# Kernel tuning notes

Measured on AMD Instinct MI355X. Metric: run time of the kernel, lower is better.

Reference implementation:

```python
import jax, jax.numpy as jnp
import numpy as np
import math

EMBED_DIM = 1024
N_HEADS = 16
HEAD_DIM = EMBED_DIM // N_HEADS  # 64


def setup_inputs() -> dict:
    key = jax.random.key(0)
    k1, k2, k3, k4, k5 = jax.random.split(key, 5)
    B, N, D, H, hd = 2, 2048, EMBED_DIM, N_HEADS, HEAD_DIM
    x = jax.random.normal(k1, (B, N, D), dtype=jnp.float32)
    # per-head kqv Linear weights, stacked: [H, D, 3*hd] (in->out layout)
    scale_in = 1.0 / math.sqrt(D)
    Wqkv = jax.random.uniform(k2, (H, D, 3 * hd), minval=-scale_in, maxval=scale_in, dtype=jnp.float32)
    bqkv = jax.random.uniform(k3, (H, 3 * hd), minval=-scale_in, maxval=scale_in, dtype=jnp.float32)
    # output projection: [D, D] (in->out layout) + bias [D]
    Wo = jax.random.uniform(k4, (D, D), minval=-scale_in, maxval=scale_in, dtype=jnp.float32)
    bo = jax.random.uniform(k5, (D,), minval=-scale_in, maxval=scale_in, dtype=jnp.float32)
    return {"x": x, "Wqkv": Wqkv, "bqkv": bqkv, "Wo": Wo, "bo": bo}


def reference(x, Wqkv, bqkv, Wo, bo):
    B, N, D = x.shape
    H, _, _ = Wqkv.shape
    hd = D // H
    # fused per-head QKV projections: [B, H, N, 3*hd]
    qkv = jnp.einsum('bnd,hdk->bhnk', x, Wqkv) + bqkv[None, :, None, :]
    k, q, v = jnp.split(qkv, 3, axis=-1)  # chunk order in source is k, q, v
    # scores: A = q @ k^T / sqrt(head_dim)  -> [B, H, N, N]
    scores = jnp.einsum('bhqd,bhkd->bhqk', q, k) / math.sqrt(hd)
    causal = jnp.tril(jnp.ones((N, N), dtype=bool))
    scores = jnp.where(causal[None, None, :, :], scores, -jnp.inf)
    attn = jax.nn.softmax(scores, axis=-1)
    sa = jnp.einsum('bhqk,bhkd->bhqd', attn, v)  # [B, H, N, hd]
    # concat heads -> [B, N, D]
    sa = sa.transpose(0, 2, 1, 3).reshape(B, N, D)
    return sa @ Wo + bo
```

## Files before the change

### kernel.cpp

```cpp
#include <hip/hip_runtime.h>
#include <stdint.h>

typedef unsigned short u16;
typedef short s16x8 __attribute__((ext_vector_type(8)));
typedef unsigned short u16x8 __attribute__((ext_vector_type(8)));
typedef unsigned int u32x4 __attribute__((ext_vector_type(4)));
typedef float f32x4 __attribute__((ext_vector_type(4)));
typedef float f32x16 __attribute__((ext_vector_type(16)));

#define GLD16(g, l) __builtin_amdgcn_global_load_lds( \
    (const __attribute__((address_space(1))) uint32_t*)(g), \
    (__attribute__((address_space(3))) uint32_t*)(l), 16, 0, 0)

__device__ __forceinline__ u16 f2bf(float f) {
  uint32_t u = __builtin_bit_cast(uint32_t, f);
  u += 0x7fffu + ((u >> 16) & 1u);
  return (u16)(u >> 16);
}

__device__ __forceinline__ uint32_t cvtpk(float lo, float hi) {
  uint32_t r;
  asm("v_cvt_pk_bf16_f32 %0, %1, %2" : "=v"(r) : "v"(lo), "v"(hi));
  return r;
}

__global__ void cvt_kernel(const float* __restrict__ in, u16* __restrict__ out) {
  int i = blockIdx.x * 256 + threadIdx.x;
  const float4* p = (const float4*)in + (size_t)i * 2;
  float4 a = p[0], b = p[1];
  u16x8 o;
  o[0] = f2bf(a.x); o[1] = f2bf(a.y); o[2] = f2bf(a.z); o[3] = f2bf(a.w);
  o[4] = f2bf(b.x); o[5] = f2bf(b.y); o[6] = f2bf(b.z); o[7] = f2bf(b.w);
  *((u16x8*)out + i) = o;
}

__global__ void transpose_f2b(const float* __restrict__ in, u16* __restrict__ out,
                              int R, int C) {
  __shared__ float tile[32][33];
  const int bz = blockIdx.z;
  in  += (size_t)bz * R * C;
  out += (size_t)bz * R * C;
  int c0 = blockIdx.x * 32, r0 = blockIdx.y * 32;
  int tx = threadIdx.x, ty = threadIdx.y;
  #pragma unroll
  for (int i = 0; i < 32; i += 8)
    tile[ty + i][tx] = in[(size_t)(r0 + ty + i) * C + c0 + tx];
  __syncthreads();
  #pragma unroll
  for (int i = 0; i < 32; i += 8)
    out[(size_t)(c0 + ty + i) * R + r0 + tx] = f2bf(tile[tx][ty + i]);
}

__global__ void transpose_b2b(const u16* __restrict__ in, u16* __restrict__ out,
                              int R, int C) {
  __shared__ u16 tile[32][33];
  const int bz = blockIdx.z;
  in  += (size_t)bz * R * C;
  out += (size_t)bz * R * C;
  int c0 = blockIdx.x * 32, r0 = blockIdx.y * 32;
  int tx = threadIdx.x, ty = threadIdx.y;
  #pragma unroll
  for (int i = 0; i < 32; i += 8)
    tile[ty + i][tx] = in[(size_t)(r0 + ty + i) * C + c0 + tx];
  __syncthreads();
  #pragma unroll
  for (int i = 0; i < 32; i += 8)
    out[(size_t)(c0 + ty + i) * R + r0 + tx] = tile[tx][ty + i];
}

template <int EPI>
__global__ __launch_bounds__(256) void gemm128(
    const u16* __restrict__ A, const u16* __restrict__ Bt, int K,
    const float* __restrict__ bias,
    u16* __restrict__ kb, u16* __restrict__ qb, u16* __restrict__ vb,
    float* __restrict__ fout) {
  __shared__ __align__(16) u16 As[128 * 64];
  __shared__ __align__(16) u16 Bs[128 * 64];
  const int tid = threadIdx.x;
  const int lane = tid & 63;
  const int wr = (tid >> 6) >> 1, wc = (tid >> 6) & 1;
  const int row0 = blockIdx.y * 128, col0 = blockIdx.x * 128;
  const int l15 = lane & 15, l4 = lane >> 4;
  const u16* Ablk = A + (size_t)row0 * K;
  const u16* Bblk = Bt + (size_t)col0 * K;
  f32x4 acc[4][4] = {};
  for (int k0 = 0; k0 < K; k0 += 64) {
    #pragma unroll
    for (int i = 0; i < 4; i++) {
      int off = (i * 256 + tid) * 8;
      int r = off >> 6, c = off & 63;
      GLD16(Ablk + (size_t)r * K + k0 + c, As + off);
    }
    #pragma unroll
    for (int i = 0; i < 4; i++) {
      int off = (i * 256 + tid) * 8;
      int r = off >> 6, c = off & 63;
      GLD16(Bblk + (size_t)r * K + k0 + c, Bs + off);
    }
    __syncthreads();
    #pragma unroll
    for (int kc = 0; kc < 2; kc++) {
      s16x8 af[4], bfr[4];
      #pragma unroll
      for (int m = 0; m < 4; m++)
        af[m] = *(const s16x8*)(As + (wr * 64 + m * 16 + l15) * 64 + kc * 32 + l4 * 8);
      #pragma unroll
      for (int n = 0; n < 4; n++)
        bfr[n] = *(const s16x8*)(Bs + (wc * 64 + n * 16 + l15) * 64 + kc * 32 + l4 * 8);
      #pragma unroll
      for (int m = 0; m < 4; m++)
        #pragma unroll
        for (int n = 0; n < 4; n++)
          acc[m][n] = __builtin_amdgcn_mfma_f32_16x16x32_bf16(af[m], bfr[n], acc[m][n], 0, 0, 0);
    }
    __syncthreads();
  }
  const int rbase = row0 + wr * 64;
  const int cbase = col0 + wc * 64;
  if (EPI == 0) {
    #pragma unroll
    for (int n = 0; n < 4; n++) {
      int c = cbase + n * 16 + l15;
      int h = c / 192, rr = c % 192;
      int part = rr >> 6, d = rr & 63;
      float bv = bias[h * 192 + rr];
      u16* dst = (part == 0) ? kb : (part == 1) ? qb : vb;
      float sc = (part == 1) ? 0.125f * 1.44269504f : 1.0f;
      #pragma unroll
      for (int m = 0; m < 4; m++)
        #pragma unroll
        for (int i = 0; i < 4; i++) {
          int r = rbase + m * 16 + l4 * 4 + i;
          int b = r >> 11, nn = r & 2047;
          dst[(((size_t)(b * 16 + h) * 2048 + nn) << 6) + d] = f2bf((acc[m][n][i] + bv) * sc);
        }
    }
  } else {
    #pragma unroll
    for (int n = 0; n < 4; n++) {
      int c = cbase + n * 16 + l15;
      float bv = bias[c];
      #pragma unroll
      for (int m = 0; m < 4; m++)
        #pragma unroll
        for (int i = 0; i < 4; i++) {
          int r = rbase + m * 16 + l4 * 4 + i;
          fout[(size_t)r * 1024 + c] = acc[m][n][i] + bv;
        }
    }
  }
}

__global__ __launch_bounds__(256, 2) void attn_kernel(
    const u16* __restrict__ q, const u16* __restrict__ k,
    const u16* __restrict__ vt, u16* __restrict__ sa) {
  __shared__ __align__(16) u16 Ks[2][64 * 64];
  __shared__ __align__(16) u16 Vs[2][64 * 64];
  __shared__ __align__(16) float Mo[2][64][36];
  __shared__ float Mml[2][64][2];
  const int tid = threadIdx.x;
  const int lane = tid & 63;
  const int wave = tid >> 6;
  const int p = wave & 1;
  const int q2 = wave >> 1;
  const int l31 = lane & 31;
  const int h = lane >> 5;

  const int bid = blockIdx.x;
  const int bh = (bid & 7) * 4 + ((bid >> 3) & 3);
  const int j = bid >> 5;
  const u16* kbh = k + (((size_t)bh * 2048) << 6);
  const u16* vbh = vt + (size_t)bh * 64 * 2048;
  const int b_ = bh >> 4, head = bh & 15;
  const int swz = (l31 & 7) << 4;

  int cur = 0;
  for (int sub = 0; sub < 2; sub++) {
    const int t = sub ? j : (31 - j);
    const int qrow = t * 64 + p * 32 + l31;

    #pragma unroll
    for (int i = 0; i < 2; i++) {
      int o2 = tid * 16 + i * 4096;
      int row = o2 >> 7;
      int cs = (o2 & 127) ^ ((row & 7) << 4);
      GLD16(kbh + (((size_t)row) << 6) + (cs >> 1), (u16*)Ks[cur] + (o2 >> 1));
      GLD16(vbh + (size_t)row * 2048 + (cs >> 1), (u16*)Vs[cur] + (o2 >> 1));
    }

    const u16* qr = q + (((size_t)bh * 2048 + qrow) << 6);
    s16x8 qf[4];
    #pragma unroll
    for (int c = 0; c < 4; c++)
      qf[c] = *(const s16x8*)(qr + c * 16 + h * 8);

    f32x16 o0 = {}, o1 = {};
    float m_ = -3e38f, l_ = 0.f;

    for (int kt = 0; kt <= t; kt++) {
      if (kt < t) {
        u16* KsB = (u16*)Ks[cur ^ 1];
        u16* VsB = (u16*)Vs[cur ^ 1];
        #pragma unroll
        for (int i = 0; i < 2; i++) {
          int o2 = tid * 16 + i * 4096;
          int row = o2 >> 7;
          int cs = (o2 & 127) ^ ((row & 7) << 4);
          GLD16(kbh + (((size_t)((kt + 1) * 64 + row)) << 6) + (cs >> 1), KsB + (o2 >> 1));
          GLD16(vbh + (size_t)row * 2048 + (kt + 1) * 64 + (cs >> 1), VsB + (o2 >> 1));
        }
        asm volatile("s_waitcnt vmcnt(4)" ::: "memory");
      } else {
        asm volatile("s_waitcnt vmcnt(0)" ::: "memory");
      }
      __builtin_amdgcn_s_barrier();
      __builtin_amdgcn_sched_barrier(0);

      const bool active = !(kt == t && q2 == 1 && p == 0);
      if (active) {
        const char* Kc = (const char*)Ks[cur];
        const char* Vc = (const char*)Vs[cur];
        f32x16 s0 = {};
        __builtin_amdgcn_s_setprio(1);
        #pragma unroll
        for (int c = 0; c < 4; c++) {
          s16x8 kf = *(const s16x8*)(Kc + (q2 * 32 + l31) * 128 + ((c * 32 + 16 * h) ^ swz));
          s0 = __builtin_amdgcn_mfma_f32_32x32x16_bf16(kf, qf[c], s0, 0, 0, 0);
        }
        __builtin_amdgcn_s_setprio(0);

        if (kt == t) {
          int kvb = t * 64 + q2 * 32 + 4 * h;
          #pragma unroll
          for (int r = 0; r < 16; r++)
            if (kvb + (r & 3) + 8 * (r >> 2) > qrow) s0[r] = -3e38f;
        }

        float pmax = s0[0];
        #pragma unroll
        for (int r = 1; r < 16; r++) pmax = fmaxf(pmax, s0[r]);
        pmax = fmaxf(pmax, __shfl_xor(pmax, 32));
        bool need = pmax > m_ + 11.f;
        if (__any((int)need)) {
          float mn = fmaxf(m_, pmax);
          float al = exp2f(m_ - mn);
          m_ = mn;
          l_ *= al;
          #pragma unroll
          for (int r = 0; r < 16; r++) { o0[r] *= al; o1[r] *= al; }
        }
        float rs = 0.f;
        #pragma unroll
        for (int r = 0; r < 16; r++) {
          float pv = exp2f(s0[r] - m_);
          s0[r] = pv;
          rs += pv;
        }
        rs += __shfl_xor(rs, 32);
        l_ += rs;

        uint32_t pk[8];
        #pragma unroll
        for (int g = 0; g < 8; g++)
          pk[g] = cvtpk(s0[2 * g], s0[2 * g + 1]);
        s16x8 pf[2];
        #pragma unroll
        for (int ss = 0; ss < 2; ss++) {
          uint32_t sendA = h ? pk[4 * ss + 0] : pk[4 * ss + 2];
          uint32_t sendB = h ? pk[4 * ss + 1] : pk[4 * ss + 3];
          uint32_t rA = (uint32_t)__shfl_xor((int)sendA, 32);
          uint32_t rB = (uint32_t)__shfl_xor((int)sendB, 32);
          u32x4 w;
          w[0] = h ? rA : pk[4 * ss + 0];
          w[1] = h ? rB : pk[4 * ss + 1];
          w[2] = h ? pk[4 * ss + 2] : rA;
          w[3] = h ? pk[4 * ss + 3] : rB;
          pf[ss] = __builtin_bit_cast(s16x8, w);
        }

        __builtin_amdgcn_s_setprio(1);
        #pragma unroll
        for (int ss = 0; ss < 2; ss++) {
          s16x8 vf0 = *(const s16x8*)(Vc + l31 * 128 + ((q2 * 64 + ss * 32 + 16 * h) ^ swz));
          s16x8 vf1 = *(const s16x8*)(Vc + (32 + l31) * 128 + ((q2 * 64 + ss * 32 + 16 * h) ^ swz));
          o0 = __builtin_amdgcn_mfma_f32_32x32x16_bf16(vf0, pf[ss], o0, 0, 0, 0);
          o1 = __builtin_amdgcn_mfma_f32_32x32x16_bf16(vf1, pf[ss], o1, 0, 0, 0);
        }
        __builtin_amdgcn_s_setprio(0);
      }
      __builtin_amdgcn_sched_barrier(0);
      __builtin_amdgcn_s_barrier();
      cur ^= 1;
    }

    if (q2) {
      float4* dst = (float4*)&Mo[p][lane][0];
      #pragma unroll
      for (int c = 0; c < 4; c++) {
        f32x4 a = {o0[4 * c], o0[4 * c + 1], o0[4 * c + 2], o0[4 * c + 3]};
        f32x4 b = {o1[4 * c], o1[4 * c + 1], o1[4 * c + 2], o1[4 * c + 3]};
        dst[c] = __builtin_bit_cast(float4, a);
        dst[4 + c] = __builtin_bit_cast(float4, b);
      }
      Mml[p][lane][0] = m_;
      Mml[p][lane][1] = l_;
    }
    __syncthreads();
    if (!q2) {
      float mB = Mml[p][lane][0], lB = Mml[p][lane][1];
      float ob[32];
      #pragma unroll
      for (int c = 0; c < 8; c++) {
        float4 v = ((const float4*)&Mo[p][lane][0])[c];
        ob[4 * c] = v.x; ob[4 * c + 1] = v.y; ob[4 * c + 2] = v.z; ob[4 * c + 3] = v.w;
      }
      float mS = fmaxf(m_, mB);
      float aA = exp2f(m_ - mS), aB = exp2f(mB - mS);
      float inv = 1.f / (l_ * aA + lB * aB);
      u16* dst = sa + ((size_t)(b_ * 2048 + qrow) << 10) + head * 64;
      #pragma unroll
      for (int i = 0; i < 8; i++) {
        int r = 2 * i;
        int d = (r & 3) + 8 * (r >> 2) + 4 * h;
        float v0 = (o0[r] * aA + ob[r] * aB) * inv;
        float v1 = (o0[r + 1] * aA + ob[r + 1] * aB) * inv;
        *(uint32_t*)(dst + d) = cvtpk(v0, v1);
        float w0 = (o1[r] * aA + ob[16 + r] * aB) * inv;
        float w1 = (o1[r + 1] * aA + ob[16 + r + 1] * aB) * inv;
        *(uint32_t*)(dst + d + 32) = cvtpk(w0, w1);
      }
    }
    __syncthreads();
  }
}

extern "C" void kernel_launch(void* const* d_in, const int* in_sizes, int n_in,
                              void* d_out, int out_size, void* d_ws, size_t ws_size,
                              hipStream_t stream) {
  const float* x    = (const float*)d_in[0];
  const float* Wqkv = (const float*)d_in[1];
  const float* bqkv = (const float*)d_in[2];
  const float* Wo   = (const float*)d_in[3];
  const float* bo   = (const float*)d_in[4];
  float* out = (float*)d_out;

  u16* xb  = (u16*)d_ws;
  u16* wqt = xb + 4194304;
  u16* wot = wqt + 3145728;
  u16* qb  = wot + 1048576;
  u16* kb  = qb + 4194304;
  u16* vb  = kb + 4194304;
  u16* vtb = vb + 4194304;
  u16* sab = xb;

  cvt_kernel<<<2048, 256, 0, stream>>>(x, xb);
  transpose_f2b<<<dim3(6, 32, 16), dim3(32, 8), 0, stream>>>(Wqkv, wqt, 1024, 192);
  transpose_f2b<<<dim3(32, 32, 1), dim3(32, 8), 0, stream>>>(Wo, wot, 1024, 1024);
  gemm128<0><<<dim3(24, 32), 256, 0, stream>>>(xb, wqt, 1024, bqkv, kb, qb, vb, nullptr);
  transpose_b2b<<<dim3(2, 64, 32), dim3(32, 8), 0, stream>>>(vb, vtb, 2048, 64);
  attn_kernel<<<dim3(512), 256, 0, stream>>>(qb, kb, vtb, sab);
  gemm128<1><<<dim3(8, 32), 256, 0, stream>>>(sab, wot, 1024, bo, nullptr, nullptr, nullptr, out);
}
```

Baseline: 214.8 us.

## Swizzle LDS, remap blocks for XCD locality, vectorize QKV epilogue, retile out GEMM

Both GEMMs now stage tiles in LDS with an XOR swizzle on the 16-byte column chunks, to cut bank conflicts on the fragment reads. Block indices are remapped so that consecutive workgroups on the same XCD share rows of the input. The QKV GEMM swaps MFMA operands so each lane holds four consecutive output columns, and writes them as packed bf16 pairs in one 8-byte store using hardware conversion. The output projection uses 128x64 tiles to launch 512 blocks instead of 256, giving more parallelism across CUs at the cost of less reuse per block.

```diff
diff --git a/kernel.cpp b/kernel.cpp
--- a/kernel.cpp
+++ b/kernel.cpp
@@ -4,6 +4,7 @@
 typedef unsigned short u16;
 typedef short s16x8 __attribute__((ext_vector_type(8)));
 typedef unsigned short u16x8 __attribute__((ext_vector_type(8)));
+typedef unsigned int u32x2 __attribute__((ext_vector_type(2)));
 typedef unsigned int u32x4 __attribute__((ext_vector_type(4)));
 typedef float f32x4 __attribute__((ext_vector_type(4)));
 typedef float f32x16 __attribute__((ext_vector_type(16)));
@@ -68,86 +69,151 @@
     out[(size_t)(c0 + ty + i) * R + r0 + tx] = tile[tx][ty + i];
 }
 
-template <int EPI>
-__global__ __launch_bounds__(256) void gemm128(
-    const u16* __restrict__ A, const u16* __restrict__ Bt, int K,
+__global__ __launch_bounds__(256) void gemm_qkv(
+    const u16* __restrict__ A, const u16* __restrict__ Bt,
     const float* __restrict__ bias,
-    u16* __restrict__ kb, u16* __restrict__ qb, u16* __restrict__ vb,
-    float* __restrict__ fout) {
+    u16* __restrict__ kb, u16* __restrict__ qb, u16* __restrict__ vb) {
   __shared__ __align__(16) u16 As[128 * 64];
   __shared__ __align__(16) u16 Bs[128 * 64];
   const int tid = threadIdx.x;
   const int lane = tid & 63;
   const int wr = (tid >> 6) >> 1, wc = (tid >> 6) & 1;
-  const int row0 = blockIdx.y * 128, col0 = blockIdx.x * 128;
   const int l15 = lane & 15, l4 = lane >> 4;
-  const u16* Ablk = A + (size_t)row0 * K;
-  const u16* Bblk = Bt + (size_t)col0 * K;
+  const int lin = blockIdx.x;
+  const int wg = (lin & 7) * 96 + (lin >> 3);
+  const int bx = wg % 24, by = wg / 24;
+  const int row0 = by * 128, col0 = bx * 128;
+  const u16* Ablk = A + (size_t)row0 * 1024;
+  const u16* Bblk = Bt + (size_t)col0 * 1024;
   f32x4 acc[4][4] = {};
-  for (int k0 = 0; k0 < K; k0 += 64) {
+  for (int k0 = 0; k0 < 1024; k0 += 64) {
     #pragma unroll
     for (int i = 0; i < 4; i++) {
-      int off = (i * 256 + tid) * 8;
-      int r = off >> 6, c = off & 63;
-      GLD16(Ablk + (size_t)r * K + k0 + c, As + off);
+      int off = (i * 256 + tid) * 16;
+      int row = off >> 7;
+      int cs = (off & 127) ^ ((row & 7) << 4);
+      GLD16(Ablk + (size_t)row * 1024 + k0 + (cs >> 1), (u16*)As + (off >> 1));
     }
     #pragma unroll
     for (int i = 0; i < 4; i++) {
-      int off = (i * 256 + tid) * 8;
-      int r = off >> 6, c = off & 63;
-      GLD16(Bblk + (size_t)r * K + k0 + c, Bs + off);
+      int off = (i * 256 + tid) * 16;
+      int row = off >> 7;
+      int cs = (off & 127) ^ ((row & 7) << 4);
+      GLD16(Bblk + (size_t)row * 1024 + k0 + (cs >> 1), (u16*)Bs + (off >> 1));
     }
     __syncthreads();
     #pragma unroll
     for (int kc = 0; kc < 2; kc++) {
-      s16x8 af[4], bfr[4];
+      s16x8 xf[4], wf[4];
+      #pragma unroll
+      for (int m = 0; m < 4; m++) {
+        int row = wr * 64 + m * 16 + l15;
+        xf[m] = *(const s16x8*)((const char*)As + row * 128 +
+                                ((kc * 64 + l4 * 16) ^ ((row & 7) << 4)));
+      }
+      #pragma unroll
+      for (int n = 0; n < 4; n++) {
+        int row = wc * 64 + n * 16 + l15;
+        wf[n] = *(const s16x8*)((const char*)Bs + row * 128 +
+                                ((kc * 64 + l4 * 16) ^ ((row & 7) << 4)));
+      }
       #pragma unroll
       for (int m = 0; m < 4; m++)
-        af[m] = *(const s16x8*)(As + (wr * 64 + m * 16 + l15) * 64 + kc * 32 + l4 * 8);
-      #pragma unroll
-      for (int n = 0; n < 4; n++)
-        bfr[n] = *(const s16x8*)(Bs + (wc * 64 + n * 16 + l15) * 64 + kc * 32 + l4 * 8);
-      #pragma unroll
-      for (int m = 0; m < 4; m++)
         #pragma unroll
         for (int n = 0; n < 4; n++)
-          acc[m][n] = __builtin_amdgcn_mfma_f32_16x16x32_bf16(af[m], bfr[n], acc[m][n], 0, 0, 0);
+          acc[m][n] = __builtin_amdgcn_mfma_f32_16x16x32_bf16(wf[n], xf[m], acc[m][n], 0, 0, 0);
     }
     __syncthreads();
   }
-  const int rbase = row0 + wr * 64;
-  const int cbase = col0 + wc * 64;
-  if (EPI == 0) {
-    #pragma unroll
-    for (int n = 0; n < 4; n++) {
-      int c = cbase + n * 16 + l15;
-      int h = c / 192, rr = c % 192;
-      int part = rr >> 6, d = rr & 63;
-      float bv = bias[h * 192 + rr];
-      u16* dst = (part == 0) ? kb : (part == 1) ? qb : vb;
-      float sc = (part == 1) ? 0.125f * 1.44269504f : 1.0f;
-      #pragma unroll
-      for (int m = 0; m < 4; m++)
-        #pragma unroll
-        for (int i = 0; i < 4; i++) {
-          int r = rbase + m * 16 + l4 * 4 + i;
-          int b = r >> 11, nn = r & 2047;
-          dst[(((size_t)(b * 16 + h) * 2048 + nn) << 6) + d] = f2bf((acc[m][n][i] + bv) * sc);
-        }
-    }
-  } else {
-    #pragma unroll
-    for (int n = 0; n < 4; n++) {
-      int c = cbase + n * 16 + l15;
-      float bv = bias[c];
-      #pragma unroll
-      for (int m = 0; m < 4; m++)
-        #pragma unroll
-        for (int i = 0; i < 4; i++) {
-          int r = rbase + m * 16 + l4 * 4 + i;
-          fout[(size_t)r * 1024 + c] = acc[m][n][i] + bv;
-        }
-    }
+  const int nng = row0 + wr * 64;
+  const int cg0 = col0 + wc * 64;
+  #pragma unroll
+  for (int n = 0; n < 4; n++) {
+    int cb = cg0 + n * 16 + l4 * 4;
+    int h = cb / 192, rr = cb % 192;
+    int part = rr >> 6, d = rr & 63;
+    u16* dst = (part == 0) ? kb : (part == 1) ? qb : vb;
+    float sc = (part == 1) ? 0.125f * 1.44269504f : 1.0f;
+    float4 bv = *(const float4*)(bias + h * 192 + rr);
+    #pragma unroll
+    for (int m = 0; m < 4; m++) {
+      int nn = nng + m * 16 + l15;
+      int b = nn >> 11, n2 = nn & 2047;
+      u16* p = dst + (((size_t)(b * 16 + h) * 2048 + n2) << 6) + d;
+      u32x2 w;
+      w[0] = cvtpk((acc[m][n][0] + bv.x) * sc, (acc[m][n][1] + bv.y) * sc);
+      w[1] = cvtpk((acc[m][n][2] + bv.z) * sc, (acc[m][n][3] + bv.w) * sc);
+      *(u32x2*)p = w;
+    }
+  }
+}
+
+__global__ __launch_bounds__(256) void gemm_out(
+    const u16* __restrict__ A, const u16* __restrict__ Bt,
+    const float* __restrict__ bias, float* __restrict__ fout) {
+  __shared__ __align__(16) u16 As[128 * 64];
+  __shared__ __align__(16) u16 Bs[64 * 64];
+  const int tid = threadIdx.x;
+  const int lane = tid & 63;
+  const int w = tid >> 6;
+  const int l15 = lane & 15, l4 = lane >> 4;
+  const int lin = blockIdx.x;
+  const int wg = (lin & 7) * 64 + (lin >> 3);
+  const int bx = wg & 15, by = wg >> 4;
+  const int row0 = by * 128, col0 = bx * 64;
+  const u16* Ablk = A + (size_t)row0 * 1024;
+  const u16* Bblk = Bt + (size_t)col0 * 1024;
+  f32x4 acc[2][4] = {};
+  for (int k0 = 0; k0 < 1024; k0 += 64) {
+    #pragma unroll
+    for (int i = 0; i < 4; i++) {
+      int off = (i * 256 + tid) * 16;
+      int row = off >> 7;
+      int cs = (off & 127) ^ ((row & 7) << 4);
+      GLD16(Ablk + (size_t)row * 1024 + k0 + (cs >> 1), (u16*)As + (off >> 1));
+    }
+    #pragma unroll
+    for (int i = 0; i < 2; i++) {
+      int off = (i * 256 + tid) * 16;
+      int row = off >> 7;
+      int cs = (off & 127) ^ ((row & 7) << 4);
+      GLD16(Bblk + (size_t)row * 1024 + k0 + (cs >> 1), (u16*)Bs + (off >> 1));
+    }
+    __syncthreads();
+    #pragma unroll
+    for (int kc = 0; kc < 2; kc++) {
+      s16x8 xf[2], wf[4];
+      #pragma unroll
+      for (int m = 0; m < 2; m++) {
+        int row = w * 32 + m * 16 + l15;
+        xf[m] = *(const s16x8*)((const char*)As + row * 128 +
+                                ((kc * 64 + l4 * 16) ^ ((row & 7) << 4)));
+      }
+      #pragma unroll
+      for (int n = 0; n < 4; n++) {
+        int row = n * 16 + l15;
+        wf[n] = *(const s16x8*)((const char*)Bs + row * 128 +
+                                ((kc * 64 + l4 * 16) ^ ((row & 7) << 4)));
+      }
+      #pragma unroll
+      for (int m = 0; m < 2; m++)
+        #pragma unroll
+        for (int n = 0; n < 4; n++)
+          acc[m][n] = __builtin_amdgcn_mfma_f32_16x16x32_bf16(xf[m], wf[n], acc[m][n], 0, 0, 0);
+    }
+    __syncthreads();
+  }
+  #pragma unroll
+  for (int n = 0; n < 4; n++) {
+    int c = col0 + n * 16 + l15;
+    float bv = bias[c];
+    #pragma unroll
+    for (int m = 0; m < 2; m++)
+      #pragma unroll
+      for (int i = 0; i < 4; i++) {
+        int r = row0 + w * 32 + m * 16 + l4 * 4 + i;
+        fout[(size_t)r * 1024 + c] = acc[m][n][i] + bv;
+      }
   }
 }
 
@@ -270,12 +336,12 @@
           uint32_t sendB = h ? pk[4 * ss + 1] : pk[4 * ss + 3];
           uint32_t rA = (uint32_t)__shfl_xor((int)sendA, 32);
           uint32_t rB = (uint32_t)__shfl_xor((int)sendB, 32);
-          u32x4 w;
-          w[0] = h ? rA : pk[4 * ss + 0];
-          w[1] = h ? rB : pk[4 * ss + 1];
-          w[2] = h ? pk[4 * ss + 2] : rA;
-          w[3] = h ? pk[4 * ss + 3] : rB;
-          pf[ss] = __builtin_bit_cast(s16x8, w);
+          u32x4 w2;
+          w2[0] = h ? rA : pk[4 * ss + 0];
+          w2[1] = h ? rB : pk[4 * ss + 1];
+          w2[2] = h ? pk[4 * ss + 2] : rA;
+          w2[3] = h ? pk[4 * ss + 3] : rB;
+          pf[ss] = __builtin_bit_cast(s16x8, w2);
         }
 
         __builtin_amdgcn_s_setprio(1);
@@ -356,8 +422,8 @@
   cvt_kernel<<<2048, 256, 0, stream>>>(x, xb);
   transpose_f2b<<<dim3(6, 32, 16), dim3(32, 8), 0, stream>>>(Wqkv, wqt, 1024, 192);
   transpose_f2b<<<dim3(32, 32, 1), dim3(32, 8), 0, stream>>>(Wo, wot, 1024, 1024);
-  gemm128<0><<<dim3(24, 32), 256, 0, stream>>>(xb, wqt, 1024, bqkv, kb, qb, vb, nullptr);
+  gemm_qkv<<<dim3(768), 256, 0, stream>>>(xb, wqt, bqkv, kb, qb, vb);
   transpose_b2b<<<dim3(2, 64, 32), dim3(32, 8), 0, stream>>>(vb, vtb, 2048, 64);
   attn_kernel<<<dim3(512), 256, 0, stream>>>(qb, kb, vtb, sab);
-  gemm128<1><<<dim3(8, 32), 256, 0, stream>>>(sab, wot, 1024, bo, nullptr, nullptr, nullptr, out);
-}
+  gemm_out<<<dim3(512), 256, 0, stream>>>(sab, wot, bo, out);
+}
```

Measured after the change: 195.8 us. 8.8% less time.
